# Optimization experiments

Hardware: AMD Instinct MI355X
Metric: run time of the kernel (lower is better)

## Reference

```python
import jax, jax.numpy as jnp
import numpy as np

B, L, D, V, d, N, H = 16, 1024, 50, 129, 64, 2, 8
DK = d // H           # 8
DFF = 2 * d           # 128
CVE = int(np.sqrt(d)) # 8
EPS = 1e-07 ** 2      # module squares epsilon
MASK_ATTN = -1e-30    # Transformer mask_value (as in source)
MASK_POOL = -1e+30    # Attention-pooling mask_value


def setup_inputs() -> dict:
    key = jax.random.key(0)
    ks = jax.random.split(key, 32)
    g = lambda i, shape, s=0.02: (jax.random.normal(ks[i], shape, dtype=jnp.float32) * s)
    inp = {
        'demo':   jax.random.normal(ks[0], (B, D), dtype=jnp.float32),
        'times':  jax.random.uniform(ks[1], (B, L), dtype=jnp.float32),
        'values': jax.random.normal(ks[2], (B, L), dtype=jnp.float32),
        'varis':  jax.random.randint(ks[3], (B, L), 0, V + 1),
        # variable embedding table
        'emb': g(4, (V + 1, d), 0.05),
        # CVE for values: Linear(1,CVE)+tanh+Linear(CVE,d,no bias)
        'vW1': g(5, (1, CVE), 0.5), 'vb1': jnp.zeros((CVE,), jnp.float32), 'vW2': g(6, (CVE, d), 0.1),
        # CVE for times
        'tW1': g(7, (1, CVE), 0.5), 'tb1': jnp.zeros((CVE,), jnp.float32), 'tW2': g(8, (CVE, d), 0.1),
        # Transformer params
        'Wq': g(9,  (N, H, d, DK), 0.1), 'Wk': g(10, (N, H, d, DK), 0.1),
        'Wv': g(11, (N, H, d, DK), 0.1), 'Wo': g(12, (N, H * DK, d), 0.1),
        'W1': g(13, (N, d, DFF), 0.1), 'b1': jnp.zeros((N, DFF), jnp.float32),
        'W2': g(14, (N, DFF, d), 0.1), 'b2': jnp.zeros((N, d), jnp.float32),
        'gamma': jnp.ones((2 * N,), jnp.float32), 'beta': jnp.zeros((2 * N,), jnp.float32),
        # Attention pooling: Linear(d,2d)+tanh+Linear(2d,1,no bias)
        'aW1': g(15, (d, 2 * d), 0.1), 'ab1': jnp.zeros((2 * d,), jnp.float32), 'aW2': g(16, (2 * d, 1), 0.1),
        # demo stack: Linear(D,2d)+tanh+Linear(2d,d)+tanh
        'dW1': g(17, (D, 2 * d), 0.1), 'db1': jnp.zeros((2 * d,), jnp.float32),
        'dW2': g(18, (2 * d, d), 0.1), 'db2': jnp.zeros((d,), jnp.float32),
        # output head: Linear(2d,1)+sigmoid+flatten
        'Wout': g(19, (2 * d, 1), 0.1), 'bout': jnp.zeros((1,), jnp.float32),
    }
    return inp


def _ln(X, g, b):
    mean = jnp.mean(X, axis=-1, keepdims=True)
    var = jnp.mean(jnp.square(X - mean), axis=-1, keepdims=True)
    return (X - mean) / jnp.sqrt(var + EPS) * g + b


def _forward(demo, times, values, varis, emb, vW1, vb1, vW2, tW1, tb1, tW2,
             Wq, Wk, Wv, Wo, W1, b1, W2, b2, gamma, beta,
             aW1, ab1, aW2, dW1, db1, dW2, db2, Wout, bout):
    mask = (varis > 0).astype(jnp.float32)  # [B,L]
    demo_enc = jnp.tanh(jnp.tanh(demo @ dW1 + db1) @ dW2 + db2)  # [B,d]
    varis_emb = emb[varis]                                       # [B,L,d]
    values_emb = jnp.tanh(values[..., None] @ vW1 + vb1) @ vW2   # [B,L,d]
    times_emb = jnp.tanh(times[..., None] @ tW1 + tb1) @ tW2     # [B,L,d]
    X = varis_emb + values_emb + times_emb

    mb = mask[:, None, None, :]  # [B,1,1,L] broadcasts over heads & query rows
    for i in range(N):
        q = jnp.einsum('bld,hdk->bhlk', X, Wq[i])
        k = jnp.einsum('bld,hdk->bhlk', X, Wk[i])
        v = jnp.einsum('bld,hdk->bhlk', X, Wv[i])
        A = jnp.einsum('bhlk,bhmk->bhlm', q, k)      # no 1/sqrt(dk) scaling (faithful)
        A = mb * A + (1.0 - mb) * MASK_ATTN
        A = jax.nn.softmax(A, axis=-1)
        O = jnp.einsum('bhlm,bhmk->bhlk', A, v)      # [B,H,L,DK]
        conc = jnp.transpose(O, (0, 2, 1, 3)).reshape(O.shape[0], O.shape[2], H * DK)
        X = X + conc @ Wo[i]
        X = _ln(X, gamma[2 * i], beta[2 * i])
        ffn = jax.nn.relu(X @ W1[i] + b1[i]) @ W2[i] + b2[i]
        X = X + ffn
        X = _ln(X, gamma[2 * i + 1], beta[2 * i + 1])

    aw = jnp.tanh(X @ aW1 + ab1) @ aW2               # [B,L,1]
    m = mask[..., None]
    aw = jax.nn.softmax(m * aw + (1.0 - m) * MASK_POOL, axis=-2)
    fused = jnp.sum(X * aw, axis=-2)                 # [B,d]
    conc = jnp.concatenate([fused, demo_enc], axis=-1)
    return jax.nn.sigmoid(conc @ Wout + bout).reshape(-1)  # [B]


def reference(demo, times, values, varis, emb, vW1, vb1, vW2, tW1, tb1, tW2,
              Wq, Wk, Wv, Wo, W1, b1, W2, b2, gamma, beta,
              aW1, ab1, aW2, dW1, db1, dW2, db2, Wout, bout):
    return _forward(demo, times, values, varis, emb, vW1, vb1, vW2, tW1, tb1, tW2,
                    Wq, Wk, Wv, Wo, W1, b1, W2, b2, gamma, beta,
                    aW1, ab1, aW2, dW1, db1, dW2, db2, Wout, bout)
```

## Files before the change

kernel.cpp:

```cpp
#include <hip/hip_runtime.h>
#include <math.h>


typedef __bf16 bf16x8 __attribute__((ext_vector_type(8)));
typedef __bf16 bf16x2 __attribute__((ext_vector_type(2)));
typedef float f32x16 __attribute__((ext_vector_type(16)));
typedef unsigned int uint4e __attribute__((ext_vector_type(4)));
typedef unsigned long long u64;

static __device__ __forceinline__ float wave_sum64(float x) {
#pragma unroll
    for (int off = 32; off > 0; off >>= 1) x += __shfl_xor(x, off, 64);
    return x;
}

static __device__ __forceinline__ unsigned pack2(float a, float b) {
    bf16x2 t; t[0] = (__bf16)a; t[1] = (__bf16)b;
    return __builtin_bit_cast(unsigned, t);
}

static __device__ __forceinline__ float exp2fast(float x) {
#if defined(__has_builtin) && __has_builtin(__builtin_amdgcn_exp2f)
    return __builtin_amdgcn_exp2f(x);
#else
    return exp2f(x);
#endif
}

static __device__ __forceinline__ void plswap(unsigned v, unsigned& lo, unsigned& hi_) {
#if defined(__has_builtin) && __has_builtin(__builtin_amdgcn_permlane32_swap)
    auto r = __builtin_amdgcn_permlane32_swap(v, v, false, false);
    lo = r[0]; hi_ = r[1];
#else
    unsigned x = __shfl_xor(v, 32, 64);
    bool h = (threadIdx.x & 32) != 0;
    lo = h ? x : v;
    hi_ = h ? v : x;
#endif
}

__global__ __launch_bounds__(256) void embed_demo_kernel(
    const float* __restrict__ times, const float* __restrict__ values,
    const int* __restrict__ varis, const float* __restrict__ emb,
    const float* __restrict__ vW1, const float* __restrict__ vb1, const float* __restrict__ vW2,
    const float* __restrict__ tW1, const float* __restrict__ tb1, const float* __restrict__ tW2,
    const float* __restrict__ demo, const float* __restrict__ dW1, const float* __restrict__ db1,
    const float* __restrict__ dW2, const float* __restrict__ db2,
    float* __restrict__ X, float* __restrict__ mask, float* __restrict__ denc)
{
    __shared__ float sh[128];
    int tid = threadIdx.x;
    if (blockIdx.x < 4096) {
        int row = blockIdx.x * 4 + (tid >> 6);
        int c   = tid & 63;
        float v = values[row];
        float t = times[row];
        int var = varis[row];
        if (c == 0) mask[row] = (var > 0) ? 1.0f : 0.0f;
        float th = 0.f;
        if (c < 8)       th = tanhf(fmaf(v, vW1[c], vb1[c]));
        else if (c < 16) th = tanhf(fmaf(t, tW1[c - 8], tb1[c - 8]));
        float acc = emb[var * 64 + c];
#pragma unroll
        for (int j = 0; j < 8; ++j) {
            acc = fmaf(__shfl(th, j, 64),     vW2[j * 64 + c], acc);
            acc = fmaf(__shfl(th, j + 8, 64), tW2[j * 64 + c], acc);
        }
        X[row * 64 + c] = acc;
    } else {
        int b = blockIdx.x - 4096;
        if (tid < 128) {
            float a = db1[tid];
            for (int j = 0; j < 50; ++j) a = fmaf(demo[b * 50 + j], dW1[j * 128 + tid], a);
            sh[tid] = tanhf(a);
        }
        __syncthreads();
        if (tid < 64) {
            float a2 = db2[tid];
#pragma unroll 8
            for (int j = 0; j < 128; ++j) a2 = fmaf(sh[j], dW2[j * 64 + tid], a2);
            denc[b * 64 + tid] = tanhf(a2);
        }
    }
}

__global__ __launch_bounds__(256) void qkv_kernel(
    const float* __restrict__ X, const float* __restrict__ mask,
    const float* __restrict__ Wq, const float* __restrict__ Wk, const float* __restrict__ Wv,
    __bf16* __restrict__ qbf, __bf16* __restrict__ kbf, __bf16* __restrict__ vtb)
{
    __shared__ __align__(16) unsigned char qsm[52224];
    float* sWq = (float*)qsm;
    float* sWk = sWq + 4352;
    float* sWv = sWk + 4352;
    int tid = threadIdx.x;
    for (int idx = tid; idx < 4096; idx += 256) {
        int h = idx >> 9, c = (idx >> 3) & 63, kk = idx & 7;
        int o = h * 8 + kk;
        sWq[o * 68 + c] = Wq[idx];
        sWk[o * 68 + c] = Wk[idx];
        sWv[o * 68 + c] = Wv[idx];
    }
    int row0 = blockIdx.x * 16;
    __syncthreads();
    int lane = tid & 63;
    int wv4 = (tid >> 6) * 4;
    float aq[4] = {0.f, 0.f, 0.f, 0.f};
    float ak[4] = {0.f, 0.f, 0.f, 0.f};
    float av[4] = {0.f, 0.f, 0.f, 0.f};
#pragma unroll
    for (int c = 0; c < 64; c += 4) {
        float4 xv[4];
#pragma unroll
        for (int rr = 0; rr < 4; ++rr)
            xv[rr] = *(const float4*)(X + (row0 + wv4 + rr) * 64 + c);
        float4 wq = *(const float4*)(sWq + lane * 68 + c);
        float4 wk = *(const float4*)(sWk + lane * 68 + c);
        float4 wvv= *(const float4*)(sWv + lane * 68 + c);
#pragma unroll
        for (int rr = 0; rr < 4; ++rr) {
            aq[rr] = fmaf(xv[rr].x, wq.x, aq[rr]);  aq[rr] = fmaf(xv[rr].y, wq.y, aq[rr]);
            aq[rr] = fmaf(xv[rr].z, wq.z, aq[rr]);  aq[rr] = fmaf(xv[rr].w, wq.w, aq[rr]);
            ak[rr] = fmaf(xv[rr].x, wk.x, ak[rr]);  ak[rr] = fmaf(xv[rr].y, wk.y, ak[rr]);
            ak[rr] = fmaf(xv[rr].z, wk.z, ak[rr]);  ak[rr] = fmaf(xv[rr].w, wk.w, ak[rr]);
            av[rr] = fmaf(xv[rr].x, wvv.x, av[rr]); av[rr] = fmaf(xv[rr].y, wvv.y, av[rr]);
            av[rr] = fmaf(xv[rr].z, wvv.z, av[rr]); av[rr] = fmaf(xv[rr].w, wvv.w, av[rr]);
        }
    }
    float aqr[4], akr[4], avr[4];
#pragma unroll
    for (int rr = 0; rr < 4; ++rr) {
        float km = mask[row0 + wv4 + rr];
        aqr[rr] = aq[rr] * 1.4426950408889634f;
        akr[rr] = (km != 0.f) ? ak[rr] : 0.f;
        avr[rr] = av[rr];
    }
    __syncthreads();
    __bf16* sQb = (__bf16*)qsm;
    __bf16* sKb = (__bf16*)(qsm + 2304);
    __bf16* sVt = (__bf16*)(qsm + 4608);
    int h = lane >> 3, kk = lane & 7;
#pragma unroll
    for (int rr = 0; rr < 4; ++rr) {
        int r = wv4 + rr;
        sQb[h * 136 + r * 8 + kk] = (__bf16)aqr[rr];
        sKb[h * 136 + r * 8 + kk] = (__bf16)akr[rr];
        sVt[lane * 18 + r] = (__bf16)avr[rr];
    }
    __syncthreads();
    int b = row0 >> 10, l0 = row0 & 1023;
    unsigned* qg = (unsigned*)qbf;
    unsigned* kg = (unsigned*)kbf;
    const unsigned* q32 = (const unsigned*)sQb;
    const unsigned* k32 = (const unsigned*)sKb;
#pragma unroll
    for (int it = 0; it < 2; ++it) {
        int idx = it * 256 + tid;
        int hh = idx >> 6, w = idx & 63;
        int gbase = ((b * 8 + hh) * 1024 + l0) * 4;
        qg[gbase + w] = q32[hh * 68 + w];
        kg[gbase + w] = k32[hh * 68 + w];
    }
#pragma unroll
    for (int it = 0; it < 2; ++it) {
        int idx = it * 256 + tid;
        int hkk = idx >> 3, lp = idx & 7;
        unsigned w = ((const unsigned*)sVt)[hkk * 9 + lp];
        int hh = hkk >> 3, k2 = hkk & 7;
        ((unsigned*)(vtb + (b * 8 + hh) * 8192 + k2 * 1024 + l0))[lp] = w;
    }
}

__global__ __launch_bounds__(256, 2) void attn_mfma_kernel(
    const __bf16* __restrict__ qbf, const __bf16* __restrict__ kbf,
    const __bf16* __restrict__ vtb, float* __restrict__ O)
{
    __shared__ __align__(16) unsigned char smem[35008];
    __bf16* sK  = (__bf16*)smem;
    __bf16* sVT = (__bf16*)(smem + 16384);

    int tid   = threadIdx.x;
    int bh    = blockIdx.x & 127;
    int chunk = blockIdx.x >> 7;

    const u64* kg = (const u64*)(kbf + bh * 8192);
    u64* sKq = (u64*)sK;
#pragma unroll
    for (int i = 0; i < 8; ++i) sKq[i * 256 + tid] = kg[i * 256 + tid];

    const u64* vgb = (const u64*)(vtb + bh * 8192);
#pragma unroll
    for (int it = 0; it < 8; ++it) {
        int idx = it * 256 + tid;
        int r = idx >> 8, w = idx & 255;
        ((u64*)(sVT + r * 1032))[w] = vgb[idx];
    }
    {
        unsigned* p1 = (unsigned*)(sVT + 8 * 1032);
        p1[tid] = 0x3f803f80u;
        p1[256 + tid] = 0x3f803f80u;
    }
    __syncthreads();

    int lane = tid & 63;
    int wv   = tid >> 6;
    int hi   = lane >> 5;
    int l31  = lane & 31;
    unsigned hm = hi ? 0u : 0xffffffffu;

    int qrow = chunk * 128 + wv * 32 + l31;

    bf16x8 qf;
    {
        const __bf16* qp = qbf + (bh * 1024 + qrow) * 8;
        uint4e qa = *(const uint4e*)qp;
        qa[0] &= hm; qa[1] &= hm; qa[2] &= hm; qa[3] &= hm;
        qf = __builtin_bit_cast(bf16x8, qa);
    }

    f32x16 acc, zc;
#pragma unroll
    for (int i = 0; i < 16; ++i) { acc[i] = 0.f; zc[i] = 0.f; }

    const bf16x8* sKv = (const bf16x8*)sK;
    const __bf16* vbase = sVT + (l31 < 8 ? l31 : 8) * 1032;

    bf16x8 kf = sKv[l31];
#pragma unroll 2
    for (int kt = 0; kt < 32; ++kt) {
        bf16x8 kfn = sKv[((kt + 1) & 31) * 32 + l31];
        f32x16 st = __builtin_amdgcn_mfma_f32_32x32x16_bf16(kf, qf, zc, 0, 0, 0);
        float p[16];
#pragma unroll
        for (int r = 0; r < 16; ++r) p[r] = exp2fast(st[r]);

#pragma unroll
        for (int h = 0; h < 2; ++h) {
            unsigned La0, Ha0, Lb0, Hb0, La1, Ha1, Lb1, Hb1;
            int g0 = 2 * h, g1 = 2 * h + 1;
            plswap(pack2(p[4 * g0 + 0], p[4 * g0 + 1]), La0, Ha0);
            plswap(pack2(p[4 * g0 + 2], p[4 * g0 + 3]), Lb0, Hb0);
            plswap(pack2(p[4 * g1 + 0], p[4 * g1 + 1]), La1, Ha1);
            plswap(pack2(p[4 * g1 + 2], p[4 * g1 + 3]), Lb1, Hb1);
            uint4e pw;
            pw[0] = hi ? La1 : La0;
            pw[1] = hi ? Lb1 : Lb0;
            pw[2] = hi ? Ha1 : Ha0;
            pw[3] = hi ? Hb1 : Hb0;
            bf16x8 vf = *(const bf16x8*)(vbase + kt * 32 + 16 * h + 8 * hi);
            acc = __builtin_amdgcn_mfma_f32_32x32x16_bf16(vf, __builtin_bit_cast(bf16x8, pw), acc, 0, 0, 0);
        }
        kf = kfn;
    }

    float inv = 1.0f / acc[4];
    __syncthreads();
    float* sO = (float*)smem;
    int qloc = wv * 32 + l31;
    float4 t0;
    t0.x = acc[0] * inv; t0.y = acc[1] * inv; t0.z = acc[2] * inv; t0.w = acc[3] * inv;
    *(float4*)(sO + qloc * 12 + 4 * hi) = t0;
    __syncthreads();
    float* og = O + (bh * 1024 + chunk * 128) * 8;
    {
        int q = tid >> 1, part = tid & 1;
        *(float4*)(og + tid * 4) = *(const float4*)(sO + q * 12 + part * 4);
    }
}

__global__ __launch_bounds__(256) void proj_ln_kernel(
    float* __restrict__ X, const float* __restrict__ O,
    const float* __restrict__ Wo, const float* __restrict__ gamma, const float* __restrict__ beta,
    int gi)
{
    __shared__ float sWo[4096];
    __shared__ float so[16][64];
    int tid = threadIdx.x;
    for (int idx = tid; idx < 4096; idx += 256) sWo[idx] = Wo[idx];
    int row0 = blockIdx.x * 16;
#pragma unroll
    for (int it = 0; it < 4; ++it) {
        int idx = it * 256 + tid;
        int r = idx >> 6, j = idx & 63;
        int grow = row0 + r;
        int b = grow >> 10, l = grow & 1023;
        int bh = b * 8 + (j >> 3);
        so[r][j] = O[(bh * 1024 + l) * 8 + (j & 7)];
    }
    __syncthreads();
    int lane = tid & 63, wv = tid >> 6;
#pragma unroll
    for (int it = 0; it < 4; ++it) {
        int r = it * 4 + wv;
        float acc = 0.f;
#pragma unroll 8
        for (int j = 0; j < 64; ++j) acc = fmaf(so[r][j], sWo[j * 64 + lane], acc);
        float x = X[(row0 + r) * 64 + lane] + acc;
        float mean = wave_sum64(x) * (1.0f / 64.0f);
        float dx = x - mean;
        float var = wave_sum64(dx * dx) * (1.0f / 64.0f);
        X[(row0 + r) * 64 + lane] = dx * rsqrtf(var + 1e-14f) * gamma[gi] + beta[gi];
    }
}

__global__ __launch_bounds__(256) void ffn_kernel(
    float* __restrict__ X, const float* __restrict__ W1, const float* __restrict__ b1,
    const float* __restrict__ W2, const float* __restrict__ b2,
    const float* __restrict__ gamma, const float* __restrict__ beta, int gi)
{
    __shared__ __align__(16) float sW[128 * 68];
    __shared__ __align__(16) float sX[2048];
    __shared__ __align__(16) float sH[32 * 132];
    int tid = threadIdx.x;
    for (int idx = tid; idx < 8192; idx += 256) {
        int c = idx >> 7, j = idx & 127;
        sW[j * 68 + c] = W1[idx];
    }
    int row0 = blockIdx.x * 32;
    for (int i = tid; i < 512; i += 256)
        ((float4*)sX)[i] = ((const float4*)(X + row0 * 64))[i];
    __syncthreads();
    {
        int j4 = tid & 31;
        int r0 = (tid >> 5) * 4;
        float acc[4][4];
#pragma unroll
        for (int jj = 0; jj < 4; ++jj) {
            float bb = b1[j4 + 32 * jj];
#pragma unroll
            for (int rr = 0; rr < 4; ++rr) acc[rr][jj] = bb;
        }
#pragma unroll 2
        for (int c = 0; c < 64; c += 4) {
            float4 xv[4];
#pragma unroll
            for (int rr = 0; rr < 4; ++rr) xv[rr] = *(const float4*)(sX + (r0 + rr) * 64 + c);
#pragma unroll
            for (int jj = 0; jj < 4; ++jj) {
                float4 wv = *(const float4*)(sW + (j4 + 32 * jj) * 68 + c);
#pragma unroll
                for (int rr = 0; rr < 4; ++rr) {
                    acc[rr][jj] = fmaf(xv[rr].x, wv.x, acc[rr][jj]);
                    acc[rr][jj] = fmaf(xv[rr].y, wv.y, acc[rr][jj]);
                    acc[rr][jj] = fmaf(xv[rr].z, wv.z, acc[rr][jj]);
                    acc[rr][jj] = fmaf(xv[rr].w, wv.w, acc[rr][jj]);
                }
            }
        }
#pragma unroll
        for (int rr = 0; rr < 4; ++rr)
#pragma unroll
            for (int jj = 0; jj < 4; ++jj)
                sH[(r0 + rr) * 132 + j4 + 32 * jj] = fmaxf(acc[rr][jj], 0.0f);
    }
    __syncthreads();
    for (int idx = tid; idx < 8192; idx += 256) {
        int j = idx >> 6, c = idx & 63;
        sW[c * 132 + j] = W2[idx];
    }
    __syncthreads();
    int c4 = tid & 15;
    int r0b = (tid >> 4) * 2;
    float acc2[2][4];
#pragma unroll
    for (int cc = 0; cc < 4; ++cc) {
        float bb = b2[c4 + 16 * cc];
        acc2[0][cc] = bb; acc2[1][cc] = bb;
    }
#pragma unroll 2
    for (int jc = 0; jc < 128; jc += 4) {
        float4 hv[2];
#pragma unroll
        for (int rr = 0; rr < 2; ++rr)
            hv[rr] = *(const float4*)(sH + (r0b + rr) * 132 + jc);
#pragma unroll
        for (int cc = 0; cc < 4; ++cc) {
            float4 wvv = *(const float4*)(sW + (c4 + 16 * cc) * 132 + jc);
#pragma unroll
            for (int rr = 0; rr < 2; ++rr) {
                acc2[rr][cc] = fmaf(hv[rr].x, wvv.x, acc2[rr][cc]);
                acc2[rr][cc] = fmaf(hv[rr].y, wvv.y, acc2[rr][cc]);
                acc2[rr][cc] = fmaf(hv[rr].z, wvv.z, acc2[rr][cc]);
                acc2[rr][cc] = fmaf(hv[rr].w, wvv.w, acc2[rr][cc]);
            }
        }
    }
    __syncthreads();
#pragma unroll
    for (int rr = 0; rr < 2; ++rr)
#pragma unroll
        for (int cc = 0; cc < 4; ++cc)
            sH[(r0b + rr) * 64 + c4 + 16 * cc] = acc2[rr][cc];
    __syncthreads();
    int lane = tid & 63, wv = tid >> 6;
#pragma unroll
    for (int it = 0; it < 8; ++it) {
        int r = wv * 8 + it;
        float x = sX[r * 64 + lane] + sH[r * 64 + lane];
        float mean = wave_sum64(x) * (1.0f / 64.0f);
        float dx = x - mean;
        float var = wave_sum64(dx * dx) * (1.0f / 64.0f);
        X[(row0 + r) * 64 + lane] = dx * rsqrtf(var + 1e-14f) * gamma[gi] + beta[gi];
    }
}

__global__ __launch_bounds__(256) void aw_kernel(
    const float* __restrict__ X, const float* __restrict__ aW1, const float* __restrict__ ab1,
    const float* __restrict__ aW2, float* __restrict__ aw)
{
    __shared__ __align__(16) float sW[128 * 68];
    __shared__ __align__(16) float sX[2048];
    int tid = threadIdx.x;
    for (int idx = tid; idx < 8192; idx += 256) {
        int c = idx >> 7, j = idx & 127;
        sW[j * 68 + c] = aW1[idx];
    }
    int row0 = blockIdx.x * 32;
    for (int i = tid; i < 512; i += 256)
        ((float4*)sX)[i] = ((const float4*)(X + row0 * 64))[i];
    __syncthreads();
    int j4 = tid & 31;
    int r0 = (tid >> 5) * 4;
    float acc[4][4];
#pragma unroll
    for (int jj = 0; jj < 4; ++jj) {
        float bb = ab1[j4 + 32 * jj];
#pragma unroll
        for (int rr = 0; rr < 4; ++rr) acc[rr][jj] = bb;
    }
#pragma unroll 2
    for (int c = 0; c < 64; c += 4) {
        float4 xv[4];
#pragma unroll
        for (int rr = 0; rr < 4; ++rr) xv[rr] = *(const float4*)(sX + (r0 + rr) * 64 + c);
#pragma unroll
        for (int jj = 0; jj < 4; ++jj) {
            float4 wv = *(const float4*)(sW + (j4 + 32 * jj) * 68 + c);
#pragma unroll
            for (int rr = 0; rr < 4; ++rr) {
                acc[rr][jj] = fmaf(xv[rr].x, wv.x, acc[rr][jj]);
                acc[rr][jj] = fmaf(xv[rr].y, wv.y, acc[rr][jj]);
                acc[rr][jj] = fmaf(xv[rr].z, wv.z, acc[rr][jj]);
                acc[rr][jj] = fmaf(xv[rr].w, wv.w, acc[rr][jj]);
            }
        }
    }
    float a2[4];
#pragma unroll
    for (int jj = 0; jj < 4; ++jj) a2[jj] = aW2[j4 + 32 * jj];
    int lane = tid & 63;
#pragma unroll
    for (int rr = 0; rr < 4; ++rr) {
        float part = tanhf(acc[rr][0]) * a2[0] + tanhf(acc[rr][1]) * a2[1]
                   + tanhf(acc[rr][2]) * a2[2] + tanhf(acc[rr][3]) * a2[3];
#pragma unroll
        for (int off = 16; off > 0; off >>= 1) part += __shfl_xor(part, off, 64);
        if ((lane & 31) == 0) aw[row0 + r0 + rr] = part;
    }
}

__global__ __launch_bounds__(1024) void pool_kernel(
    const float* __restrict__ X, const float* __restrict__ aw, const float* __restrict__ mask,
    const float* __restrict__ denc, const float* __restrict__ Wout,
    const float* __restrict__ bout, float* __restrict__ out)
{
    __shared__ float sp[1024];
    __shared__ float red[16];
    __shared__ float red2[16];
    __shared__ float sf[16][64];
    int b = blockIdx.x, tid = threadIdx.x;
    float s = (mask[b * 1024 + tid] != 0.0f) ? aw[b * 1024 + tid] : -1e30f;
    float m = s;
#pragma unroll
    for (int off = 32; off > 0; off >>= 1) m = fmaxf(m, __shfl_xor(m, off, 64));
    if ((tid & 63) == 0) red[tid >> 6] = m;
    __syncthreads();
    float gmax = red[0];
#pragma unroll
    for (int i = 1; i < 16; ++i) gmax = fmaxf(gmax, red[i]);
    float p = __expf(s - gmax);
    sp[tid] = p;
    float psum = wave_sum64(p);
    if ((tid & 63) == 0) red2[tid >> 6] = psum;
    __syncthreads();
    float tot = 0.f;
#pragma unroll
    for (int i = 0; i < 16; ++i) tot += red2[i];
    float inv = 1.0f / tot;
    int c = tid & 63, g = tid >> 6;
    int l0 = g * 64;
    float f = 0.f;
#pragma unroll 4
    for (int i = 0; i < 64; ++i)
        f = fmaf(sp[l0 + i], X[(b * 1024 + l0 + i) * 64 + c], f);
    sf[g][c] = f;
    __syncthreads();
    if (tid < 64) {
        float fc = 0.f;
#pragma unroll
        for (int ch = 0; ch < 16; ++ch) fc += sf[ch][tid];
        fc *= inv;
        float contrib = fc * Wout[tid] + denc[b * 64 + tid] * Wout[64 + tid];
        contrib = wave_sum64(contrib);
        if (tid == 0) out[b] = 1.0f / (1.0f + __expf(-(contrib + bout[0])));
    }
}

extern "C" void kernel_launch(void* const* d_in, const int* in_sizes, int n_in,
                              void* d_out, int out_size, void* d_ws, size_t ws_size,
                              hipStream_t stream)
{
    const float* demo  = (const float*)d_in[0];
    const float* times = (const float*)d_in[1];
    const float* values= (const float*)d_in[2];
    const int*   varis = (const int*)d_in[3];
    const float* emb   = (const float*)d_in[4];
    const float* vW1   = (const float*)d_in[5];
    const float* vb1   = (const float*)d_in[6];
    const float* vW2   = (const float*)d_in[7];
    const float* tW1   = (const float*)d_in[8];
    const float* tb1   = (const float*)d_in[9];
    const float* tW2   = (const float*)d_in[10];
    const float* Wq    = (const float*)d_in[11];
    const float* Wk    = (const float*)d_in[12];
    const float* Wv    = (const float*)d_in[13];
    const float* Wo    = (const float*)d_in[14];
    const float* W1    = (const float*)d_in[15];
    const float* b1    = (const float*)d_in[16];
    const float* W2    = (const float*)d_in[17];
    const float* b2    = (const float*)d_in[18];
    const float* gamma = (const float*)d_in[19];
    const float* beta  = (const float*)d_in[20];
    const float* aW1   = (const float*)d_in[21];
    const float* ab1   = (const float*)d_in[22];
    const float* aW2   = (const float*)d_in[23];
    const float* dW1   = (const float*)d_in[24];
    const float* db1   = (const float*)d_in[25];
    const float* dW2   = (const float*)d_in[26];
    const float* db2   = (const float*)d_in[27];
    const float* Wout  = (const float*)d_in[28];
    const float* bout  = (const float*)d_in[29];
    float* out = (float*)d_out;

    float* ws     = (float*)d_ws;
    float* X      = ws;
    float* mask   = X + 1048576;
    __bf16* qbf   = (__bf16*)(mask + 16384);
    __bf16* kbf   = qbf + 1048576;
    __bf16* vtb   = kbf + 1048576;
    float* Ob     = (float*)(vtb + 1048576);
    float* awb    = Ob + 1048576;
    float* denc   = awb + 16384;

    embed_demo_kernel<<<4112, 256, 0, stream>>>(times, values, varis, emb, vW1, vb1, vW2,
                                                tW1, tb1, tW2, demo, dW1, db1, dW2, db2,
                                                X, mask, denc);
    for (int i = 0; i < 2; ++i) {
        qkv_kernel<<<1024, 256, 0, stream>>>(X, mask, Wq + i * 4096, Wk + i * 4096, Wv + i * 4096,
                                             qbf, kbf, vtb);
        attn_mfma_kernel<<<1024, 256, 0, stream>>>(qbf, kbf, vtb, Ob);
        proj_ln_kernel<<<1024, 256, 0, stream>>>(X, Ob, Wo + i * 4096, gamma, beta, 2 * i);
        ffn_kernel<<<512, 256, 0, stream>>>(X, W1 + i * 8192, b1 + i * 128, W2 + i * 8192,
                                            b2 + i * 64, gamma, beta, 2 * i + 1);
    }
    aw_kernel<<<512, 256, 0, stream>>>(X, aW1, ab1, aW2, awb);
    pool_kernel<<<16, 1024, 0, stream>>>(X, awb, mask, denc, Wout, bout, out);
}
```

Baseline: 171.7 us.

## Fuse output projection, LayerNorm, FFN and attention pooling scores into one tail kernel

Merges proj_ln_kernel, ffn_kernel and (on the last layer) aw_kernel into a single tail_kernel that processes 32 rows per block and keeps X in shared memory across stages. The fusion removes two kernel launches per layer plus one more at the end, along with the global round trips of X between them. The cost is a longer per-block sequence of weight loads into shared memory with extra barriers, and the Wo projection is redone with a register-tiled layout.

```diff
diff --git a/kernel.cpp b/kernel.cpp
--- a/kernel.cpp
+++ b/kernel.cpp
@@ -268,57 +268,76 @@
     }
 }
 
-__global__ __launch_bounds__(256) void proj_ln_kernel(
-    float* __restrict__ X, const float* __restrict__ O,
-    const float* __restrict__ Wo, const float* __restrict__ gamma, const float* __restrict__ beta,
-    int gi)
+__global__ __launch_bounds__(256) void tail_kernel(
+    float* __restrict__ X, const float* __restrict__ O, const float* __restrict__ Wo,
+    const float* __restrict__ W1, const float* __restrict__ b1,
+    const float* __restrict__ W2, const float* __restrict__ b2,
+    const float* __restrict__ gamma, const float* __restrict__ beta, int gi,
+    const float* __restrict__ aW1, const float* __restrict__ ab1,
+    const float* __restrict__ aW2, float* __restrict__ aw, int doAw)
 {
-    __shared__ float sWo[4096];
-    __shared__ float so[16][64];
+    __shared__ __align__(16) float sW[128 * 68];
+    __shared__ __align__(16) float sX[2048];
+    __shared__ __align__(16) float sH[32 * 132];
     int tid = threadIdx.x;
-    for (int idx = tid; idx < 4096; idx += 256) sWo[idx] = Wo[idx];
-    int row0 = blockIdx.x * 16;
-#pragma unroll
-    for (int it = 0; it < 4; ++it) {
+    int row0 = blockIdx.x * 32;
+    int lane = tid & 63, wvv = tid >> 6;
+
+    for (int idx = tid; idx < 4096; idx += 256) {
+        int j = idx >> 6, c = idx & 63;
+        sW[c * 68 + j] = Wo[idx];
+    }
+#pragma unroll
+    for (int it = 0; it < 8; ++it) {
         int idx = it * 256 + tid;
         int r = idx >> 6, j = idx & 63;
         int grow = row0 + r;
         int b = grow >> 10, l = grow & 1023;
         int bh = b * 8 + (j >> 3);
-        so[r][j] = O[(bh * 1024 + l) * 8 + (j & 7)];
-    }
-    __syncthreads();
-    int lane = tid & 63, wv = tid >> 6;
-#pragma unroll
-    for (int it = 0; it < 4; ++it) {
-        int r = it * 4 + wv;
-        float acc = 0.f;
-#pragma unroll 8
-        for (int j = 0; j < 64; ++j) acc = fmaf(so[r][j], sWo[j * 64 + lane], acc);
-        float x = X[(row0 + r) * 64 + lane] + acc;
+        sH[r * 68 + j] = O[(bh * 1024 + l) * 8 + (j & 7)];
+    }
+    for (int i = tid; i < 512; i += 256)
+        ((float4*)sX)[i] = ((const float4*)(X + row0 * 64))[i];
+    __syncthreads();
+
+    {
+        int c4 = tid & 15, r0b = (tid >> 4) * 2;
+        float acc[2][4] = {{0.f,0.f,0.f,0.f},{0.f,0.f,0.f,0.f}};
+#pragma unroll 2
+        for (int j = 0; j < 64; j += 4) {
+            float4 hv0 = *(const float4*)(sH + r0b * 68 + j);
+            float4 hv1 = *(const float4*)(sH + (r0b + 1) * 68 + j);
+#pragma unroll
+            for (int cc = 0; cc < 4; ++cc) {
+                float4 wv = *(const float4*)(sW + (c4 + 16 * cc) * 68 + j);
+                acc[0][cc] = fmaf(hv0.x, wv.x, acc[0][cc]); acc[0][cc] = fmaf(hv0.y, wv.y, acc[0][cc]);
+                acc[0][cc] = fmaf(hv0.z, wv.z, acc[0][cc]); acc[0][cc] = fmaf(hv0.w, wv.w, acc[0][cc]);
+                acc[1][cc] = fmaf(hv1.x, wv.x, acc[1][cc]); acc[1][cc] = fmaf(hv1.y, wv.y, acc[1][cc]);
+                acc[1][cc] = fmaf(hv1.z, wv.z, acc[1][cc]); acc[1][cc] = fmaf(hv1.w, wv.w, acc[1][cc]);
+            }
+        }
+#pragma unroll
+        for (int rr = 0; rr < 2; ++rr)
+#pragma unroll
+            for (int cc = 0; cc < 4; ++cc)
+                sX[(r0b + rr) * 64 + c4 + 16 * cc] += acc[rr][cc];
+    }
+    __syncthreads();
+#pragma unroll
+    for (int it = 0; it < 8; ++it) {
+        int r = wvv * 8 + it;
+        float x = sX[r * 64 + lane];
         float mean = wave_sum64(x) * (1.0f / 64.0f);
         float dx = x - mean;
         float var = wave_sum64(dx * dx) * (1.0f / 64.0f);
-        X[(row0 + r) * 64 + lane] = dx * rsqrtf(var + 1e-14f) * gamma[gi] + beta[gi];
-    }
-}
-
-__global__ __launch_bounds__(256) void ffn_kernel(
-    float* __restrict__ X, const float* __restrict__ W1, const float* __restrict__ b1,
-    const float* __restrict__ W2, const float* __restrict__ b2,
-    const float* __restrict__ gamma, const float* __restrict__ beta, int gi)
-{
-    __shared__ __align__(16) float sW[128 * 68];
-    __shared__ __align__(16) float sX[2048];
-    __shared__ __align__(16) float sH[32 * 132];
-    int tid = threadIdx.x;
+        sX[r * 64 + lane] = dx * rsqrtf(var + 1e-14f) * gamma[gi] + beta[gi];
+    }
+    __syncthreads();
+
     for (int idx = tid; idx < 8192; idx += 256) {
         int c = idx >> 7, j = idx & 127;
         sW[j * 68 + c] = W1[idx];
     }
-    int row0 = blockIdx.x * 32;
-    for (int i = tid; i < 512; i += 256)
-        ((float4*)sX)[i] = ((const float4*)(X + row0 * 64))[i];
     __syncthreads();
     {
         int j4 = tid & 31;
@@ -375,13 +394,13 @@
             hv[rr] = *(const float4*)(sH + (r0b + rr) * 132 + jc);
 #pragma unroll
         for (int cc = 0; cc < 4; ++cc) {
-            float4 wvv = *(const float4*)(sW + (c4 + 16 * cc) * 132 + jc);
+            float4 wvv2 = *(const float4*)(sW + (c4 + 16 * cc) * 132 + jc);
 #pragma unroll
             for (int rr = 0; rr < 2; ++rr) {
-                acc2[rr][cc] = fmaf(hv[rr].x, wvv.x, acc2[rr][cc]);
-                acc2[rr][cc] = fmaf(hv[rr].y, wvv.y, acc2[rr][cc]);
-                acc2[rr][cc] = fmaf(hv[rr].z, wvv.z, acc2[rr][cc]);
-                acc2[rr][cc] = fmaf(hv[rr].w, wvv.w, acc2[rr][cc]);
+                acc2[rr][cc] = fmaf(hv[rr].x, wvv2.x, acc2[rr][cc]);
+                acc2[rr][cc] = fmaf(hv[rr].y, wvv2.y, acc2[rr][cc]);
+                acc2[rr][cc] = fmaf(hv[rr].z, wvv2.z, acc2[rr][cc]);
+                acc2[rr][cc] = fmaf(hv[rr].w, wvv2.w, acc2[rr][cc]);
             }
         }
     }
@@ -392,70 +411,63 @@
         for (int cc = 0; cc < 4; ++cc)
             sH[(r0b + rr) * 64 + c4 + 16 * cc] = acc2[rr][cc];
     __syncthreads();
-    int lane = tid & 63, wv = tid >> 6;
 #pragma unroll
     for (int it = 0; it < 8; ++it) {
-        int r = wv * 8 + it;
+        int r = wvv * 8 + it;
         float x = sX[r * 64 + lane] + sH[r * 64 + lane];
         float mean = wave_sum64(x) * (1.0f / 64.0f);
         float dx = x - mean;
         float var = wave_sum64(dx * dx) * (1.0f / 64.0f);
-        X[(row0 + r) * 64 + lane] = dx * rsqrtf(var + 1e-14f) * gamma[gi] + beta[gi];
-    }
-}
-
-__global__ __launch_bounds__(256) void aw_kernel(
-    const float* __restrict__ X, const float* __restrict__ aW1, const float* __restrict__ ab1,
-    const float* __restrict__ aW2, float* __restrict__ aw)
-{
-    __shared__ __align__(16) float sW[128 * 68];
-    __shared__ __align__(16) float sX[2048];
-    int tid = threadIdx.x;
+        float xo = dx * rsqrtf(var + 1e-14f) * gamma[gi + 1] + beta[gi + 1];
+        X[(row0 + r) * 64 + lane] = xo;
+        if (doAw) sX[r * 64 + lane] = xo;
+    }
+    if (!doAw) return;
+
+    __syncthreads();
     for (int idx = tid; idx < 8192; idx += 256) {
         int c = idx >> 7, j = idx & 127;
         sW[j * 68 + c] = aW1[idx];
     }
-    int row0 = blockIdx.x * 32;
-    for (int i = tid; i < 512; i += 256)
-        ((float4*)sX)[i] = ((const float4*)(X + row0 * 64))[i];
-    __syncthreads();
-    int j4 = tid & 31;
-    int r0 = (tid >> 5) * 4;
-    float acc[4][4];
-#pragma unroll
-    for (int jj = 0; jj < 4; ++jj) {
-        float bb = ab1[j4 + 32 * jj];
-#pragma unroll
-        for (int rr = 0; rr < 4; ++rr) acc[rr][jj] = bb;
-    }
+    __syncthreads();
+    {
+        int j4 = tid & 31;
+        int r0 = (tid >> 5) * 4;
+        float acc[4][4];
+#pragma unroll
+        for (int jj = 0; jj < 4; ++jj) {
+            float bb = ab1[j4 + 32 * jj];
+#pragma unroll
+            for (int rr = 0; rr < 4; ++rr) acc[rr][jj] = bb;
+        }
 #pragma unroll 2
-    for (int c = 0; c < 64; c += 4) {
-        float4 xv[4];
-#pragma unroll
-        for (int rr = 0; rr < 4; ++rr) xv[rr] = *(const float4*)(sX + (r0 + rr) * 64 + c);
-#pragma unroll
-        for (int jj = 0; jj < 4; ++jj) {
-            float4 wv = *(const float4*)(sW + (j4 + 32 * jj) * 68 + c);
-#pragma unroll
-            for (int rr = 0; rr < 4; ++rr) {
-                acc[rr][jj] = fmaf(xv[rr].x, wv.x, acc[rr][jj]);
-                acc[rr][jj] = fmaf(xv[rr].y, wv.y, acc[rr][jj]);
-                acc[rr][jj] = fmaf(xv[rr].z, wv.z, acc[rr][jj]);
-                acc[rr][jj] = fmaf(xv[rr].w, wv.w, acc[rr][jj]);
+        for (int c = 0; c < 64; c += 4) {
+            float4 xv[4];
+#pragma unroll
+            for (int rr = 0; rr < 4; ++rr) xv[rr] = *(const float4*)(sX + (r0 + rr) * 64 + c);
+#pragma unroll
+            for (int jj = 0; jj < 4; ++jj) {
+                float4 wv = *(const float4*)(sW + (j4 + 32 * jj) * 68 + c);
+#pragma unroll
+                for (int rr = 0; rr < 4; ++rr) {
+                    acc[rr][jj] = fmaf(xv[rr].x, wv.x, acc[rr][jj]);
+                    acc[rr][jj] = fmaf(xv[rr].y, wv.y, acc[rr][jj]);
+                    acc[rr][jj] = fmaf(xv[rr].z, wv.z, acc[rr][jj]);
+                    acc[rr][jj] = fmaf(xv[rr].w, wv.w, acc[rr][jj]);
+                }
             }
         }
-    }
-    float a2[4];
-#pragma unroll
-    for (int jj = 0; jj < 4; ++jj) a2[jj] = aW2[j4 + 32 * jj];
-    int lane = tid & 63;
-#pragma unroll
-    for (int rr = 0; rr < 4; ++rr) {
-        float part = tanhf(acc[rr][0]) * a2[0] + tanhf(acc[rr][1]) * a2[1]
-                   + tanhf(acc[rr][2]) * a2[2] + tanhf(acc[rr][3]) * a2[3];
-#pragma unroll
-        for (int off = 16; off > 0; off >>= 1) part += __shfl_xor(part, off, 64);
-        if ((lane & 31) == 0) aw[row0 + r0 + rr] = part;
+        float a2[4];
+#pragma unroll
+        for (int jj = 0; jj < 4; ++jj) a2[jj] = aW2[j4 + 32 * jj];
+#pragma unroll
+        for (int rr = 0; rr < 4; ++rr) {
+            float part = tanhf(acc[rr][0]) * a2[0] + tanhf(acc[rr][1]) * a2[1]
+                       + tanhf(acc[rr][2]) * a2[2] + tanhf(acc[rr][3]) * a2[3];
+#pragma unroll
+            for (int off = 16; off > 0; off >>= 1) part += __shfl_xor(part, off, 64);
+            if ((lane & 31) == 0) aw[row0 + r0 + rr] = part;
+        }
     }
 }
 
@@ -559,10 +571,10 @@
         qkv_kernel<<<1024, 256, 0, stream>>>(X, mask, Wq + i * 4096, Wk + i * 4096, Wv + i * 4096,
                                              qbf, kbf, vtb);
         attn_mfma_kernel<<<1024, 256, 0, stream>>>(qbf, kbf, vtb, Ob);
-        proj_ln_kernel<<<1024, 256, 0, stream>>>(X, Ob, Wo + i * 4096, gamma, beta, 2 * i);
-        ffn_kernel<<<512, 256, 0, stream>>>(X, W1 + i * 8192, b1 + i * 128, W2 + i * 8192,
-                                            b2 + i * 64, gamma, beta, 2 * i + 1);
-    }
-    aw_kernel<<<512, 256, 0, stream>>>(X, aW1, ab1, aW2, awb);
+        tail_kernel<<<512, 256, 0, stream>>>(X, Ob, Wo + i * 4096,
+                                             W1 + i * 8192, b1 + i * 128, W2 + i * 8192, b2 + i * 64,
+                                             gamma, beta, 2 * i,
+                                             aW1, ab1, aW2, awb, (i == 1) ? 1 : 0);
+    }
     pool_kernel<<<16, 1024, 0, stream>>>(X, awb, mask, denc, Wout, bout, out);
 }
```

After: 161.5 us. 6.0% less time.
